# Kernel optimization log

Hardware: AMD Instinct MI355X
Metric: run time of the kernel (lower is better)

Reference implementation:

```python
import jax, jax.numpy as jnp
import numpy as np

DIM = 512
HEADS = 8
DEPTH = DIM // HEADS
DFF = 2048
EPS = 1e-3  # keras BatchNormalization default epsilon


def _dense_params(key, d_in, d_out, bias=True):
    k1, k2 = jax.random.split(key)
    lim = 1.0 / np.sqrt(d_in)
    W = jax.random.uniform(k1, (d_in, d_out), minval=-lim, maxval=lim, dtype=jnp.float32)
    if bias:
        b = jnp.zeros((d_out,), jnp.float32)
        return W, b
    return W


def _bn_params(key, d):
    k1, k2 = jax.random.split(key)
    gamma = 1.0 + 0.1 * jax.random.normal(k1, (d,), jnp.float32)
    beta = 0.1 * jax.random.normal(k2, (d,), jnp.float32)
    mean = 0.05 * jax.random.normal(jax.random.fold_in(key, 7), (d,), jnp.float32)
    var = jnp.ones((d,), jnp.float32)
    return gamma, beta, mean, var


def setup_inputs() -> dict:
    key = jax.random.key(0)
    ks = jax.random.split(key, 20)
    B, S_dec, S_enc = 32, 384, 384
    inp = {
        'enc_output': jax.random.normal(ks[0], (B, S_enc, DIM), jnp.float32),
        'x2': jax.random.normal(ks[1], (B, S_dec, DIM), jnp.float32),
    }
    # mha1 (self-attn) params
    for i, nm in enumerate(['q1', 'k1', 'v1', 'o1']):
        W, b = _dense_params(ks[2 + i], DIM, DIM)
        inp[f'W{nm}'], inp[f'b{nm}'] = W, b
    # mha2 (cross-attn) params
    for i, nm in enumerate(['q2', 'k2', 'v2', 'o2']):
        W, b = _dense_params(ks[6 + i], DIM, DIM)
        inp[f'W{nm}'], inp[f'b{nm}'] = W, b
    # FFN
    inp['Wff1'] = _dense_params(ks[10], DIM, DFF, bias=False)
    inp['Wff2'] = _dense_params(ks[11], DFF, DIM, bias=False)
    # 4 batchnorms
    for i in range(1, 5):
        g, be, m, v = _bn_params(ks[11 + i], DIM)
        inp[f'bn{i}_gamma'], inp[f'bn{i}_beta'] = g, be
        inp[f'bn{i}_mean'], inp[f'bn{i}_var'] = m, v
    return inp


def _split_heads(x):
    B, S, _ = x.shape
    return x.reshape(B, S, HEADS, DEPTH).transpose(0, 2, 1, 3)


def _mha(q_in, k_in, v_in, Wq, bq, Wk, bk, Wv, bv, Wo, bo, causal):
    q = _split_heads(q_in @ Wq + bq)
    k = _split_heads(k_in @ Wk + bk)
    v = _split_heads(v_in @ Wv + bv)
    logits = jnp.einsum('bhqd,bhkd->bhqk', q, k) / jnp.sqrt(jnp.float32(DEPTH))
    if causal:
        Sq, Sk = logits.shape[-2], logits.shape[-1]
        mask = jnp.tril(jnp.ones((Sq, Sk), bool))
        logits = jnp.where(mask, logits, jnp.finfo(logits.dtype).min)
    attn = jax.nn.softmax(logits, axis=-1)
    out = jnp.einsum('bhqk,bhkd->bhqd', attn, v)
    B, _, S, _ = out.shape
    out = out.transpose(0, 2, 1, 3).reshape(B, S, DIM)
    return out @ Wo + bo


def _bn(x, gamma, beta, mean, var):
    return (x - mean) * jax.lax.rsqrt(var + EPS) * gamma + beta


def reference(enc_output, x2,
              Wq1, bq1, Wk1, bk1, Wv1, bv1, Wo1, bo1,
              Wq2, bq2, Wk2, bk2, Wv2, bv2, Wo2, bo2,
              Wff1, Wff2,
              bn1_gamma, bn1_beta, bn1_mean, bn1_var,
              bn2_gamma, bn2_beta, bn2_mean, bn2_var,
              bn3_gamma, bn3_beta, bn3_mean, bn3_var,
              bn4_gamma, bn4_beta, bn4_mean, bn4_var):
    # self-attention with causal mask (dropout = identity)
    x = _mha(x2, x2, x2, Wq1, bq1, Wk1, bk1, Wv1, bv1, Wo1, bo1, causal=True)
    x = x + x2
    xn = _bn(x, bn1_gamma, bn1_beta, bn1_mean, bn1_var)
    y = _bn(enc_output, bn2_gamma, bn2_beta, bn2_mean, bn2_var)
    # cross-attention (no mask); residual adds x2 (as in source)
    x = _mha(xn, y, y, Wq2, bq2, Wk2, bk2, Wv2, bv2, Wo2, bo2, causal=False)
    x = x + x2
    cross_out = x
    x = _bn(x, bn3_gamma, bn3_beta, bn3_mean, bn3_var)
    x = jax.nn.relu(x @ Wff1) @ Wff2
    x = x + cross_out
    x = _bn(x, bn4_gamma, bn4_beta, bn4_mean, bn4_var)
    return x
```

## Files before the change

kernel.cpp:

```cpp
#include <hip/hip_runtime.h>
#include <cstdint>
#include <cstddef>

typedef __bf16 bf16;
typedef __bf16 bf16x8 __attribute__((ext_vector_type(8)));
typedef __bf16 bf16x4 __attribute__((ext_vector_type(4)));
typedef float  f32x4  __attribute__((ext_vector_type(4)));

#define B_   32
#define S_   384
#define D_   512
#define H_   8
#define DH_  64
#define DFF_ 2048
#define NTOK (B_*S_)

__device__ __forceinline__ void gload16(const void* g, void* l){
  __builtin_amdgcn_global_load_lds((__attribute__((address_space(1))) uint32_t*)(g),
                                   (__attribute__((address_space(3))) uint32_t*)(l), 16, 0, 0);
}

struct PrepArgs { const float* w8[8]; const float* wff1; const float* wff2; const float* bn[16]; };
__global__ __launch_bounds__(256) void prep_all(PrepArgs pa, bf16* Wt8, bf16* Wff1t, bf16* Wff2t,
                                                float* sc, float* sh){
  __shared__ float t[64][65];
  int id = blockIdx.x;
  if (id < 1024){
    const float* src; bf16* dst; int R, C, tr, tc;
    if (id < 512){
      int w = id >> 6, tl = id & 63;
      src = pa.w8[w]; dst = Wt8 + (size_t)w*262144; R = 512; C = 512;
      tr = (tl>>3)*64; tc = (tl&7)*64;
    } else if (id < 768){
      int tl = id - 512;
      src = pa.wff1; dst = Wff1t; R = 512; C = 2048;
      tr = (tl>>5)*64; tc = (tl&31)*64;
    } else {
      int tl = id - 768;
      src = pa.wff2; dst = Wff2t; R = 2048; C = 512;
      tr = (tl>>3)*64; tc = (tl&7)*64;
    }
    for (int i=threadIdx.x; i<4096; i+=256){ int r=i>>6, c=i&63; t[r][c] = src[(size_t)(tr+r)*C + tc+c]; }
    __syncthreads();
    for (int i=threadIdx.x; i<4096; i+=256){ int c=i>>6, r=i&63; dst[(size_t)(tc+c)*R + tr+r] = (bf16)t[r][c]; }
  } else {
    int t2 = id - 1024;
    int i = t2 >> 1, half = t2 & 1;
    int n = half*256 + threadIdx.x;
    float g = pa.bn[i*4+0][n], b = pa.bn[i*4+1][n], m = pa.bn[i*4+2][n], v = pa.bn[i*4+3][n];
    float s = g * rsqrtf(v + 1e-3f);
    sc[i*512+n] = s; sh[i*512+n] = b - m*s;
  }
}

__global__ __launch_bounds__(256) void cvt2(const float* __restrict__ enc, const float* __restrict__ x2,
                                            const float* __restrict__ sc, const float* __restrict__ sh,
                                            bf16* __restrict__ E2, bf16* __restrict__ X2b){
  size_t e0 = ((size_t)blockIdx.x*256 + threadIdx.x)*4;
  if (blockIdx.y == 0){
    int n0 = (int)(e0 & (D_-1));
    f32x4 xv = *(const f32x4*)(enc + e0);
    bf16x4 ov;
    #pragma unroll
    for (int j=0;j<4;j++) ov[j] = (bf16)(xv[j]*sc[n0+j] + sh[n0+j]);
    *(bf16x4*)(E2 + e0) = ov;
  } else {
    f32x4 xv = *(const f32x4*)(x2 + e0);
    bf16x4 ov;
    #pragma unroll
    for (int j=0;j<4;j++) ov[j] = (bf16)xv[j];
    *(bf16x4*)(X2b + e0) = ov;
  }
}

__global__ __launch_bounds__(256,3) void gemm_bt(
    const bf16* __restrict__ A, const bf16* __restrict__ Wt,
    const float* __restrict__ b0,
    const bf16* __restrict__ residb,
    const float* __restrict__ bsc, const float* __restrict__ bsh,
    bf16* __restrict__ o0, bf16* __restrict__ o1b,
    bf16* __restrict__ vt, int vseg,
    float* __restrict__ of, bf16* __restrict__ pre,
    int M, int N, int K, int relu, int mode)
{
  __shared__ bf16 As[2][64*64];
  __shared__ bf16 Bs[2][128*64];
  int nwg = gridDim.x;
  int cpx = nwg >> 3;
  int bid = blockIdx.x;
  int swz = (bid & 7)*cpx + (bid >> 3);
  int tiles_n = N >> 7;
  int tm = swz / tiles_n, tn = swz - tm*tiles_n;

  int tid = threadIdx.x, wave = tid>>6, lane = tid&63;
  int lhi = lane>>4, llo = lane&15;
  int lrow = lane>>3, lcol = lane&7;
  int wr = wave>>1, wc = wave&1;

  f32x4 acc[2][4];
  #pragma unroll
  for (int i=0;i<2;i++)
    #pragma unroll
    for (int j=0;j<4;j++) acc[i][j] = (f32x4){0.f,0.f,0.f,0.f};

  const bf16* Abase = A  + (size_t)(tm*64)  * K;
  const bf16* Bbase = Wt + (size_t)(tn*128) * K;

  int arow0 = wave*16, brow0 = wave*32;

  auto STAGE = [&](int buf, int kt){
    #pragma unroll
    for (int q=0;q<2;q++){
      int r = arow0 + q*8 + lrow;
      int s = lcol ^ (r&7);
      gload16(Abase + (size_t)r*K + kt + s*8, (char*)&As[buf][0] + wave*2048 + q*1024);
    }
    #pragma unroll
    for (int q=0;q<4;q++){
      int r = brow0 + q*8 + lrow;
      int s = lcol ^ (r&7);
      gload16(Bbase + (size_t)r*K + kt + s*8, (char*)&Bs[buf][0] + wave*4096 + q*1024);
    }
  };

  STAGE(0, 0);
  __syncthreads();
  int nt = K >> 6;
  int cur = 0;
  for (int t=0; t<nt; ++t){
    if (t+1 < nt) STAGE(cur^1, (t+1)<<6);
    #pragma unroll
    for (int ks=0; ks<2; ks++){
      bf16x8 af[2], bfr[4];
      #pragma unroll
      for (int i=0;i<2;i++){
        int row = wr*32 + i*16 + llo;
        int slot = (ks*4 + lhi) ^ (row&7);
        af[i] = *(const bf16x8*)&As[cur][row*64 + slot*8];
      }
      #pragma unroll
      for (int j=0;j<4;j++){
        int row = wc*64 + j*16 + llo;
        int slot = (ks*4 + lhi) ^ (row&7);
        bfr[j] = *(const bf16x8*)&Bs[cur][row*64 + slot*8];
      }
      #pragma unroll
      for (int i=0;i<2;i++)
        #pragma unroll
        for (int j=0;j<4;j++)
          acc[i][j] = __builtin_amdgcn_mfma_f32_16x16x32_bf16(af[i], bfr[j], acc[i][j], 0,0,0);
    }
    __syncthreads();
    cur ^= 1;
  }

  int m0 = tm*64 + wr*32, n0 = tn*128 + wc*64;
  #pragma unroll
  for (int i=0;i<2;i++){
    #pragma unroll
    for (int j=0;j<4;j++){
      int gn = n0 + j*16 + llo;
      float vv[4];
      #pragma unroll
      for (int rr=0;rr<4;rr++){
        int gm = m0 + i*16 + lhi*4 + rr;
        float v = acc[i][j][rr];
        if (b0) v += b0[gn & 511];
        if (residb) v += (float)residb[(size_t)gm*N + gn];
        vv[rr] = v;
      }
      int gm0 = m0 + i*16 + lhi*4;
      if (mode == 1){
        int seg = gn >> 9, cn = gn & 511;
        int h = cn >> 6, dd = cn & 63;
        int bb = gm0 / S_, ss0 = gm0 - bb*S_;
        if (seg == vseg){
          bf16x4 v4;
          #pragma unroll
          for (int rr=0;rr<4;rr++) v4[rr] = (bf16)vv[rr];
          *(bf16x4*)&vt[((size_t)(bb*H_ + h)*DH_ + dd)*S_ + ss0] = v4;
        } else {
          bf16* hp = (seg == 0) ? o0 : o1b;
          #pragma unroll
          for (int rr=0;rr<4;rr++)
            hp[(((size_t)(bb*H_ + h))*S_ + ss0 + rr)*DH_ + dd] = (bf16)vv[rr];
        }
      } else {
        #pragma unroll
        for (int rr=0;rr<4;rr++){
          int gm = gm0 + rr;
          float v = vv[rr];
          if (pre)  pre[(size_t)gm*N + gn] = (bf16)v;
          if (bsc)  v = v*bsc[gn & 511] + bsh[gn & 511];
          if (relu) v = fmaxf(v, 0.f);
          if (of) of[(size_t)gm*N + gn] = v;
          else    o0[(size_t)gm*N + gn] = (bf16)v;
        }
      }
    }
  }
}

__global__ __launch_bounds__(256,3) void gemm_bt2(
    const bf16* __restrict__ A, const bf16* __restrict__ A2, int tnA,
    const bf16* __restrict__ Wt,
    const float* __restrict__ b0, const float* __restrict__ b1, const float* __restrict__ b2,
    const bf16* __restrict__ residb,
    const float* __restrict__ bsc, const float* __restrict__ bsh,
    bf16* __restrict__ o0, bf16* __restrict__ o1b,
    bf16* __restrict__ vt, int vseg,
    float* __restrict__ of,
    int M, int N, int K, int relu, int mode)
{
  __shared__ bf16 As[3][128*32];
  __shared__ bf16 Bs[3][128*32];
  int nwg = gridDim.x;
  int cpx = nwg >> 3;
  int bid = blockIdx.x;
  int swz = (bid & 7)*cpx + (bid >> 3);
  int tiles_n = N >> 7;
  int tm = swz / tiles_n, tn = swz - tm*tiles_n;

  int tid = threadIdx.x, wave = tid>>6, lane = tid&63;
  int lhi = lane>>4, llo = lane&15;
  int srow = lane>>2, sslot = lane&3;
  int wr = wave>>1, wc = wave&1;

  f32x4 acc[4][4];
  #pragma unroll
  for (int i=0;i<4;i++)
    #pragma unroll
    for (int j=0;j<4;j++) acc[i][j] = (f32x4){0.f,0.f,0.f,0.f};

  const bf16* Asrc = (A2 && tn >= tnA) ? A2 : A;
  const bf16* Abase = Asrc + (size_t)(tm*128) * K;
  const bf16* Bbase = Wt   + (size_t)(tn*128) * K;

  auto STAGE = [&](int buf, int kt){
    #pragma unroll
    for (int q=0;q<2;q++){
      int r = wave*32 + q*16 + srow;
      int s = sslot ^ ((r>>1)&3);
      gload16(Abase + (size_t)r*K + kt + s*8, (char*)&As[buf][0] + wave*2048 + q*1024);
    }
    #pragma unroll
    for (int q=0;q<2;q++){
      int r = wave*32 + q*16 + srow;
      int s = sslot ^ ((r>>1)&3);
      gload16(Bbase + (size_t)r*K + kt + s*8, (char*)&Bs[buf][0] + wave*2048 + q*1024);
    }
  };

  int nt = K >> 5;
  STAGE(0, 0);
  STAGE(1, 32);
  int cur = 0, st = 2;
  for (int t=0; t<nt; ++t){
    if (t+1 < nt) asm volatile("s_waitcnt vmcnt(4)" ::: "memory");
    else          asm volatile("s_waitcnt vmcnt(0)" ::: "memory");
    __builtin_amdgcn_s_barrier();
    asm volatile("" ::: "memory");
    if (t+2 < nt){
      STAGE(st, (t+2)<<5);
      st = (st==2) ? 0 : st+1;
    }
    bf16x8 af[4], bfr[4];
    #pragma unroll
    for (int i=0;i<4;i++){
      int row = wr*64 + i*16 + llo;
      int slot = lhi ^ ((row>>1)&3);
      af[i] = *(const bf16x8*)&As[cur][row*32 + slot*8];
    }
    #pragma unroll
    for (int j=0;j<4;j++){
      int row = wc*64 + j*16 + llo;
      int slot = lhi ^ ((row>>1)&3);
      bfr[j] = *(const bf16x8*)&Bs[cur][row*32 + slot*8];
    }
    #pragma unroll
    for (int i=0;i<4;i++)
      #pragma unroll
      for (int j=0;j<4;j++)
        acc[i][j] = __builtin_amdgcn_mfma_f32_16x16x32_bf16(af[i], bfr[j], acc[i][j], 0,0,0);
    cur = (cur==2) ? 0 : cur+1;
  }

  int m0 = tm*128 + wr*64, n0 = tn*128 + wc*64;
  #pragma unroll
  for (int i=0;i<4;i++){
    #pragma unroll
    for (int j=0;j<4;j++){
      int gn = n0 + j*16 + llo;
      float vv[4];
      #pragma unroll
      for (int rr=0;rr<4;rr++){
        int gm = m0 + i*16 + lhi*4 + rr;
        float v = acc[i][j][rr];
        if (b0){
          const float* bp = (gn < 512) ? b0 : ((gn < 1024) ? b1 : b2);
          v += bp[gn & 511];
        }
        if (residb) v += (float)residb[(size_t)gm*N + gn];
        vv[rr] = v;
      }
      int gm0 = m0 + i*16 + lhi*4;
      if (mode == 1){
        int seg = gn >> 9, cn = gn & 511;
        int h = cn >> 6, dd = cn & 63;
        int bb = gm0 / S_, ss0 = gm0 - bb*S_;
        if (seg == vseg){
          bf16x4 v4;
          #pragma unroll
          for (int rr=0;rr<4;rr++) v4[rr] = (bf16)vv[rr];
          *(bf16x4*)&vt[((size_t)(bb*H_ + h)*DH_ + dd)*S_ + ss0] = v4;
        } else {
          bf16* hp = (seg == 0) ? o0 : o1b;
          #pragma unroll
          for (int rr=0;rr<4;rr++)
            hp[(((size_t)(bb*H_ + h))*S_ + ss0 + rr)*DH_ + dd] = (bf16)vv[rr];
        }
      } else {
        #pragma unroll
        for (int rr=0;rr<4;rr++){
          int gm = gm0 + rr;
          float v = vv[rr];
          if (bsc)  v = v*bsc[gn & 511] + bsh[gn & 511];
          if (relu) v = fmaxf(v, 0.f);
          if (of) of[(size_t)gm*N + gn] = v;
          else    o0[(size_t)gm*N + gn] = (bf16)v;
        }
      }
    }
  }
}

__global__ __launch_bounds__(256,4) void attn(
    const bf16* __restrict__ Q, const bf16* __restrict__ Kx,
    const bf16* __restrict__ Vt, bf16* __restrict__ out, int causal)
{
  __shared__ bf16 Ks[64*64];
  __shared__ bf16 Vs[64*64];
  __shared__ bf16 Ps[4][16*64];
  int bid = blockIdx.x;
  int bh = bid & 255;
  int qb = bid >> 8;
  int b = bh >> 3, h = bh & 7;
  int tid = threadIdx.x, wave = tid>>6, lane = tid&63;
  int lhi = lane>>4, llo = lane&15;
  int l7 = llo & 7;
  const bf16* Qb = Q  + (size_t)bh*S_*DH_;
  const bf16* Kb = Kx + (size_t)bh*S_*DH_;
  const bf16* Vb = Vt + (size_t)bh*DH_*S_;

  bf16x8 qf[2];
  #pragma unroll
  for (int f=0; f<2; f++)
    qf[f] = *(const bf16x8*)&Qb[(size_t)(qb*64 + wave*16 + llo)*DH_ + f*32 + lhi*8];

  f32x4 oacc[4];
  #pragma unroll
  for (int f=0; f<4; f++) oacc[f] = (f32x4){0.f,0.f,0.f,0.f};
  float mrow[4], lrow4[4];
  #pragma unroll
  for (int r=0;r<4;r++){ mrow[r] = -1e9f; lrow4[r] = 0.f; }

  int KT = causal ? (qb+1) : (S_/64);

  int srow0 = tid>>3, sslot = tid&7;
  bf16x8 kreg[2], vreg[2];

  auto issue = [&](int kb){
    const bf16* kt0 = Kb + (size_t)kb*64*DH_;
    #pragma unroll
    for (int s=0;s<2;s++){
      int row = s*32 + srow0;
      kreg[s] = *(const bf16x8*)&kt0[(size_t)row*64 + sslot*8];
      vreg[s] = *(const bf16x8*)&Vb[(size_t)row*S_ + (size_t)kb*64 + sslot*8];
    }
  };
  issue(0);

  for (int kb=0; kb<KT; kb++){
    #pragma unroll
    for (int s=0;s<2;s++){
      int row = s*32 + srow0;
      int sl = sslot ^ (row&7);
      *(bf16x8*)&Ks[row*64 + sl*8] = kreg[s];
      *(bf16x8*)&Vs[row*64 + sl*8] = vreg[s];
    }
    __syncthreads();

    f32x4 sc[4];
    #pragma unroll
    for (int f=0; f<4; f++){
      f32x4 z = (f32x4){0.f,0.f,0.f,0.f};
      #pragma unroll
      for (int ks=0; ks<2; ks++){
        int row = f*16 + llo;
        int slot = (ks*4 + lhi) ^ (row&7);
        bf16x8 kf = *(const bf16x8*)&Ks[row*64 + slot*8];
        z = __builtin_amdgcn_mfma_f32_16x16x32_bf16(qf[ks], kf, z, 0,0,0);
      }
      sc[f] = z;
    }
    #pragma unroll
    for (int f=0; f<4; f++)
      #pragma unroll
      for (int r=0;r<4;r++){
        float v = sc[f][r]*0.125f;
        if (causal && kb==KT-1){
          int gcol = kb*64 + f*16 + llo;
          int grow = qb*64 + wave*16 + lhi*4 + r;
          if (gcol > grow) v = -1e9f;
        }
        sc[f][r] = v;
      }

    float alpha[4], psum[4];
    #pragma unroll
    for (int r=0;r<4;r++){
      float vm = fmaxf(fmaxf(sc[0][r],sc[1][r]), fmaxf(sc[2][r],sc[3][r]));
      #pragma unroll
      for (int msk=1; msk<16; msk<<=1) vm = fmaxf(vm, __shfl_xor(vm, msk));
      float mn = fmaxf(mrow[r], vm);
      alpha[r] = __expf(mrow[r]-mn);
      mrow[r]  = mn;
      psum[r]  = 0.f;
    }
    #pragma unroll
    for (int f=0; f<4; f++)
      #pragma unroll
      for (int r=0;r<4;r++){
        float p = __expf(sc[f][r]-mrow[r]);
        psum[r] += p;
        int row = lhi*4 + r;
        int slot = (f*2 + (llo>>3)) ^ (row&7);
        Ps[wave][row*64 + slot*8 + l7] = (bf16)p;
      }
    #pragma unroll
    for (int r=0;r<4;r++){
      float s = psum[r];
      #pragma unroll
      for (int msk=1; msk<16; msk<<=1) s += __shfl_xor(s, msk);
      lrow4[r] = lrow4[r]*alpha[r] + s;
      #pragma unroll
      for (int f=0; f<4; f++) oacc[f][r] *= alpha[r];
    }

    if (kb+1 < KT) issue(kb+1);

    asm volatile("s_waitcnt lgkmcnt(0)" ::: "memory");
    __builtin_amdgcn_sched_barrier(0);

    #pragma unroll
    for (int ks=0; ks<2; ks++){
      int pslot = (ks*4 + lhi) ^ l7;
      bf16x8 pf = *(const bf16x8*)&Ps[wave][llo*64 + pslot*8];
      #pragma unroll
      for (int f2=0; f2<4; f2++){
        int row = f2*16 + llo;
        int slot = (ks*4 + lhi) ^ (row&7);
        bf16x8 vf = *(const bf16x8*)&Vs[row*64 + slot*8];
        oacc[f2] = __builtin_amdgcn_mfma_f32_16x16x32_bf16(pf, vf, oacc[f2], 0,0,0);
      }
    }
    __syncthreads();
  }

  int qg = qb*64 + wave*16;
  #pragma unroll
  for (int f2=0; f2<4; f2++)
    #pragma unroll
    for (int r=0;r<4;r++){
      int row = qg + lhi*4 + r;
      int dd  = f2*16 + llo;
      out[((size_t)(b*S_ + row))*D_ + h*DH_ + dd] = (bf16)(oacc[f2][r] / lrow4[r]);
    }
}

extern "C" void kernel_launch(void* const* d_in, const int* in_sizes, int n_in,
                              void* d_out, int out_size, void* d_ws, size_t ws_size,
                              hipStream_t stream)
{
  (void)in_sizes; (void)n_in; (void)out_size; (void)ws_size;
  const float* enc = (const float*)d_in[0];
  const float* x2  = (const float*)d_in[1];
  const float* bq1 = (const float*)d_in[3];
  const float* bk1 = (const float*)d_in[5];
  const float* bv1 = (const float*)d_in[7];
  const float* bo1 = (const float*)d_in[9];
  const float* bq2 = (const float*)d_in[11];
  const float* bk2 = (const float*)d_in[13];
  const float* bv2 = (const float*)d_in[15];
  const float* bo2 = (const float*)d_in[17];
  float* outp = (float*)d_out;

  char* ws = (char*)d_ws;
  size_t off = 0;
  auto alloc = [&](size_t bytes)->void*{ void* p = ws + off; off += (bytes+255)&~(size_t)255; return p; };
  bf16* Wt8   = (bf16*)alloc((size_t)8*512*512*2);
  bf16* Wff1t = (bf16*)alloc((size_t)DFF_*D_*2);
  bf16* Wff2t = (bf16*)alloc((size_t)D_*DFF_*2);
  float* bnsc = (float*)alloc(4*512*4);
  float* bnsh = (float*)alloc(4*512*4);
  size_t actB = (size_t)NTOK*D_*2;
  bf16* X2b  = (bf16*)alloc(actB);
  bf16* Abuf = (bf16*)alloc(actB);
  bf16* Bbuf = (bf16*)alloc(actB);
  bf16* Cbuf = (bf16*)alloc(actB);
  bf16* Dv   = (bf16*)alloc(actB);
  bf16* E1   = (bf16*)alloc(actB);
  bf16* E2   = (bf16*)alloc(actB);
  bf16* E3   = E2;
  bf16* Fbuf = Abuf;

  bf16* Wtq1 = Wt8 + 0*262144;
  bf16* Wto1 = Wt8 + 3*262144;
  bf16* Wtq2 = Wt8 + 4*262144;
  bf16* Wto2 = Wt8 + 7*262144;

  PrepArgs pa;
  pa.w8[0]=(const float*)d_in[2];  pa.w8[1]=(const float*)d_in[4];
  pa.w8[2]=(const float*)d_in[6];  pa.w8[3]=(const float*)d_in[8];
  pa.w8[4]=(const float*)d_in[10]; pa.w8[5]=(const float*)d_in[12];
  pa.w8[6]=(const float*)d_in[14]; pa.w8[7]=(const float*)d_in[16];
  pa.wff1=(const float*)d_in[18];  pa.wff2=(const float*)d_in[19];
  for (int i=0;i<16;i++) pa.bn[i] = (const float*)d_in[20+i];
  prep_all<<<1032,256,0,stream>>>(pa, Wt8, Wff1t, Wff2t, bnsc, bnsh);
  cvt2<<<dim3(NTOK*D_/4/256, 2),256,0,stream>>>(enc, x2, bnsc+512, bnsh+512, E2, X2b);

  auto gemm = [&](const bf16* Am, const bf16* W, const float* bb0,
                  const bf16* residb, const float* sc, const float* sh,
                  bf16* oo0, float* of, bf16* pre, int N, int K, int relu){
    gemm_bt<<<(NTOK/64)*(N/128), 256, 0, stream>>>(Am, W, bb0, residb, sc, sh,
                                                   oo0, nullptr, nullptr, -1, of, pre,
                                                   NTOK, N, K, relu, 0);
  };
  auto gemm2 = [&](const bf16* Am, const bf16* A2, int tnA, const bf16* W,
                   const float* bb0, const float* bb1, const float* bb2,
                   const bf16* residb, const float* sc, const float* sh,
                   bf16* oo0, bf16* oo1, bf16* vt, int vseg, float* of,
                   int N, int K, int relu, int mode){
    gemm_bt2<<<(NTOK/128)*(N/128), 256, 0, stream>>>(Am, A2, tnA, W, bb0, bb1, bb2,
                                                     residb, sc, sh, oo0, oo1, vt, vseg, of,
                                                     NTOK, N, K, relu, mode);
  };

  gemm2(X2b, nullptr, 0, Wtq1, bq1, bk1, bv1, nullptr, nullptr, nullptr,
        Abuf, Bbuf, Dv, 2, nullptr, 1536, 512, 0, 1);
  attn<<<(S_/64)*B_*H_, 256, 0, stream>>>(Abuf, Bbuf, Dv, Cbuf, 1);
  gemm(Cbuf, Wto1, bo1, X2b, bnsc+0, bnsh+0, E1, nullptr, nullptr, 512, 512, 0);

  gemm2(E1, E2, 4, Wtq2, bq2, bk2, bv2, nullptr, nullptr, nullptr,
        Abuf, Bbuf, Dv, 2, nullptr, 1536, 512, 0, 1);
  attn<<<(S_/64)*B_*H_, 256, 0, stream>>>(Abuf, Bbuf, Dv, Cbuf, 0);
  gemm(Cbuf, Wto2, bo2, X2b, bnsc+2*512, bnsh+2*512, E1, nullptr, E3, 512, 512, 0);

  gemm2(E1, nullptr, 0, Wff1t, nullptr, nullptr, nullptr, nullptr, nullptr, nullptr,
        Fbuf, nullptr, nullptr, -1, nullptr, DFF_, 512, 1, 0);
  gemm2(Fbuf, nullptr, 0, Wff2t, nullptr, nullptr, nullptr, E3, bnsc+3*512, bnsh+3*512,
        nullptr, nullptr, nullptr, -1, outp, 512, DFF_, 0, 0);
}
```

Before: 334.9 us.

## Simplify gemm kernels: double-buffer gemm_bt2, route FFN2 through 64-row gemm_bt

Splits the epilogues so gemm_bt handles only row-major outputs with residual, batchnorm and fp32 output, while gemm_bt2 handles only the QKV/FFN1 paths. gemm_bt2 moves from a triple-buffered LDS pipeline with manual vmcnt waits to a simpler double buffer with __syncthreads, which cuts LDS use so launch bounds can go up to 4 blocks per CU. The FFN2 GEMM (K=2048, N=512) now runs on the 64x128-tile gemm_bt, which launches more workgroups. The cost is less prefetch depth in gemm_bt2, so global load latency may be exposed more often.

```diff
diff --git a/kernel.cpp b/kernel.cpp
--- a/kernel.cpp
+++ b/kernel.cpp
@@ -78,10 +78,9 @@
     const float* __restrict__ b0,
     const bf16* __restrict__ residb,
     const float* __restrict__ bsc, const float* __restrict__ bsh,
-    bf16* __restrict__ o0, bf16* __restrict__ o1b,
-    bf16* __restrict__ vt, int vseg,
+    bf16* __restrict__ o0,
     float* __restrict__ of, bf16* __restrict__ pre,
-    int M, int N, int K, int relu, int mode)
+    int M, int N, int K, int relu)
 {
   __shared__ bf16 As[2][64*64];
   __shared__ bf16 Bs[2][128*64];
@@ -160,13 +159,112 @@
     #pragma unroll
     for (int j=0;j<4;j++){
       int gn = n0 + j*16 + llo;
-      float vv[4];
       #pragma unroll
       for (int rr=0;rr<4;rr++){
         int gm = m0 + i*16 + lhi*4 + rr;
         float v = acc[i][j][rr];
         if (b0) v += b0[gn & 511];
         if (residb) v += (float)residb[(size_t)gm*N + gn];
+        if (pre)  pre[(size_t)gm*N + gn] = (bf16)v;
+        if (bsc)  v = v*bsc[gn & 511] + bsh[gn & 511];
+        if (relu) v = fmaxf(v, 0.f);
+        if (of) of[(size_t)gm*N + gn] = v;
+        else    o0[(size_t)gm*N + gn] = (bf16)v;
+      }
+    }
+  }
+}
+
+__global__ __launch_bounds__(256,4) void gemm_bt2(
+    const bf16* __restrict__ A, const bf16* __restrict__ A2, int tnA,
+    const bf16* __restrict__ Wt,
+    const float* __restrict__ b0, const float* __restrict__ b1, const float* __restrict__ b2,
+    bf16* __restrict__ o0, bf16* __restrict__ o1b,
+    bf16* __restrict__ vt, int vseg,
+    int M, int N, int K, int relu, int mode)
+{
+  __shared__ bf16 As[2][128*32];
+  __shared__ bf16 Bs[2][128*32];
+  int nwg = gridDim.x;
+  int cpx = nwg >> 3;
+  int bid = blockIdx.x;
+  int swz = (bid & 7)*cpx + (bid >> 3);
+  int tiles_n = N >> 7;
+  int tm = swz / tiles_n, tn = swz - tm*tiles_n;
+
+  int tid = threadIdx.x, wave = tid>>6, lane = tid&63;
+  int lhi = lane>>4, llo = lane&15;
+  int srow = lane>>2, sslot = lane&3;
+  int wr = wave>>1, wc = wave&1;
+
+  f32x4 acc[4][4];
+  #pragma unroll
+  for (int i=0;i<4;i++)
+    #pragma unroll
+    for (int j=0;j<4;j++) acc[i][j] = (f32x4){0.f,0.f,0.f,0.f};
+
+  const bf16* Asrc = (A2 && tn >= tnA) ? A2 : A;
+  const bf16* Abase = Asrc + (size_t)(tm*128) * K;
+  const bf16* Bbase = Wt   + (size_t)(tn*128) * K;
+
+  auto STAGE = [&](int buf, int kt){
+    #pragma unroll
+    for (int q=0;q<2;q++){
+      int r = wave*32 + q*16 + srow;
+      int s = sslot ^ ((r>>1)&3);
+      gload16(Abase + (size_t)r*K + kt + s*8, (char*)&As[buf][0] + wave*2048 + q*1024);
+    }
+    #pragma unroll
+    for (int q=0;q<2;q++){
+      int r = wave*32 + q*16 + srow;
+      int s = sslot ^ ((r>>1)&3);
+      gload16(Bbase + (size_t)r*K + kt + s*8, (char*)&Bs[buf][0] + wave*2048 + q*1024);
+    }
+  };
+
+  STAGE(0, 0);
+  __syncthreads();
+  int nt = K >> 5;
+  int cur = 0;
+  for (int t=0; t<nt; ++t){
+    if (t+1 < nt) STAGE(cur^1, (t+1)<<5);
+    bf16x8 af[4], bfr[4];
+    #pragma unroll
+    for (int i=0;i<4;i++){
+      int row = wr*64 + i*16 + llo;
+      int slot = lhi ^ ((row>>1)&3);
+      af[i] = *(const bf16x8*)&As[cur][row*32 + slot*8];
+    }
+    #pragma unroll
+    for (int j=0;j<4;j++){
+      int row = wc*64 + j*16 + llo;
+      int slot = lhi ^ ((row>>1)&3);
+      bfr[j] = *(const bf16x8*)&Bs[cur][row*32 + slot*8];
+    }
+    #pragma unroll
+    for (int i=0;i<4;i++)
+      #pragma unroll
+      for (int j=0;j<4;j++)
+        acc[i][j] = __builtin_amdgcn_mfma_f32_16x16x32_bf16(af[i], bfr[j], acc[i][j], 0,0,0);
+    __syncthreads();
+    cur ^= 1;
+  }
+
+  int m0 = tm*128 + wr*64, n0 = tn*128 + wc*64;
+  #pragma unroll
+  for (int i=0;i<4;i++){
+    #pragma unroll
+    for (int j=0;j<4;j++){
+      int gn = n0 + j*16 + llo;
+      float vv[4];
+      #pragma unroll
+      for (int rr=0;rr<4;rr++){
+        int gm = m0 + i*16 + lhi*4 + rr;
+        float v = acc[i][j][rr];
+        if (b0){
+          const float* bp = (gn < 512) ? b0 : ((gn < 1024) ? b1 : b2);
+          v += bp[gn & 511];
+        }
         vv[rr] = v;
       }
       int gm0 = m0 + i*16 + lhi*4;
@@ -190,144 +288,8 @@
         for (int rr=0;rr<4;rr++){
           int gm = gm0 + rr;
           float v = vv[rr];
-          if (pre)  pre[(size_t)gm*N + gn] = (bf16)v;
-          if (bsc)  v = v*bsc[gn & 511] + bsh[gn & 511];
           if (relu) v = fmaxf(v, 0.f);
-          if (of) of[(size_t)gm*N + gn] = v;
-          else    o0[(size_t)gm*N + gn] = (bf16)v;
-        }
-      }
-    }
-  }
-}
-
-__global__ __launch_bounds__(256,3) void gemm_bt2(
-    const bf16* __restrict__ A, const bf16* __restrict__ A2, int tnA,
-    const bf16* __restrict__ Wt,
-    const float* __restrict__ b0, const float* __restrict__ b1, const float* __restrict__ b2,
-    const bf16* __restrict__ residb,
-    const float* __restrict__ bsc, const float* __restrict__ bsh,
-    bf16* __restrict__ o0, bf16* __restrict__ o1b,
-    bf16* __restrict__ vt, int vseg,
-    float* __restrict__ of,
-    int M, int N, int K, int relu, int mode)
-{
-  __shared__ bf16 As[3][128*32];
-  __shared__ bf16 Bs[3][128*32];
-  int nwg = gridDim.x;
-  int cpx = nwg >> 3;
-  int bid = blockIdx.x;
-  int swz = (bid & 7)*cpx + (bid >> 3);
-  int tiles_n = N >> 7;
-  int tm = swz / tiles_n, tn = swz - tm*tiles_n;
-
-  int tid = threadIdx.x, wave = tid>>6, lane = tid&63;
-  int lhi = lane>>4, llo = lane&15;
-  int srow = lane>>2, sslot = lane&3;
-  int wr = wave>>1, wc = wave&1;
-
-  f32x4 acc[4][4];
-  #pragma unroll
-  for (int i=0;i<4;i++)
-    #pragma unroll
-    for (int j=0;j<4;j++) acc[i][j] = (f32x4){0.f,0.f,0.f,0.f};
-
-  const bf16* Asrc = (A2 && tn >= tnA) ? A2 : A;
-  const bf16* Abase = Asrc + (size_t)(tm*128) * K;
-  const bf16* Bbase = Wt   + (size_t)(tn*128) * K;
-
-  auto STAGE = [&](int buf, int kt){
-    #pragma unroll
-    for (int q=0;q<2;q++){
-      int r = wave*32 + q*16 + srow;
-      int s = sslot ^ ((r>>1)&3);
-      gload16(Abase + (size_t)r*K + kt + s*8, (char*)&As[buf][0] + wave*2048 + q*1024);
-    }
-    #pragma unroll
-    for (int q=0;q<2;q++){
-      int r = wave*32 + q*16 + srow;
-      int s = sslot ^ ((r>>1)&3);
-      gload16(Bbase + (size_t)r*K + kt + s*8, (char*)&Bs[buf][0] + wave*2048 + q*1024);
-    }
-  };
-
-  int nt = K >> 5;
-  STAGE(0, 0);
-  STAGE(1, 32);
-  int cur = 0, st = 2;
-  for (int t=0; t<nt; ++t){
-    if (t+1 < nt) asm volatile("s_waitcnt vmcnt(4)" ::: "memory");
-    else          asm volatile("s_waitcnt vmcnt(0)" ::: "memory");
-    __builtin_amdgcn_s_barrier();
-    asm volatile("" ::: "memory");
-    if (t+2 < nt){
-      STAGE(st, (t+2)<<5);
-      st = (st==2) ? 0 : st+1;
-    }
-    bf16x8 af[4], bfr[4];
-    #pragma unroll
-    for (int i=0;i<4;i++){
-      int row = wr*64 + i*16 + llo;
-      int slot = lhi ^ ((row>>1)&3);
-      af[i] = *(const bf16x8*)&As[cur][row*32 + slot*8];
-    }
-    #pragma unroll
-    for (int j=0;j<4;j++){
-      int row = wc*64 + j*16 + llo;
-      int slot = lhi ^ ((row>>1)&3);
-      bfr[j] = *(const bf16x8*)&Bs[cur][row*32 + slot*8];
-    }
-    #pragma unroll
-    for (int i=0;i<4;i++)
-      #pragma unroll
-      for (int j=0;j<4;j++)
-        acc[i][j] = __builtin_amdgcn_mfma_f32_16x16x32_bf16(af[i], bfr[j], acc[i][j], 0,0,0);
-    cur = (cur==2) ? 0 : cur+1;
-  }
-
-  int m0 = tm*128 + wr*64, n0 = tn*128 + wc*64;
-  #pragma unroll
-  for (int i=0;i<4;i++){
-    #pragma unroll
-    for (int j=0;j<4;j++){
-      int gn = n0 + j*16 + llo;
-      float vv[4];
-      #pragma unroll
-      for (int rr=0;rr<4;rr++){
-        int gm = m0 + i*16 + lhi*4 + rr;
-        float v = acc[i][j][rr];
-        if (b0){
-          const float* bp = (gn < 512) ? b0 : ((gn < 1024) ? b1 : b2);
-          v += bp[gn & 511];
-        }
-        if (residb) v += (float)residb[(size_t)gm*N + gn];
-        vv[rr] = v;
-      }
-      int gm0 = m0 + i*16 + lhi*4;
-      if (mode == 1){
-        int seg = gn >> 9, cn = gn & 511;
-        int h = cn >> 6, dd = cn & 63;
-        int bb = gm0 / S_, ss0 = gm0 - bb*S_;
-        if (seg == vseg){
-          bf16x4 v4;
-          #pragma unroll
-          for (int rr=0;rr<4;rr++) v4[rr] = (bf16)vv[rr];
-          *(bf16x4*)&vt[((size_t)(bb*H_ + h)*DH_ + dd)*S_ + ss0] = v4;
-        } else {
-          bf16* hp = (seg == 0) ? o0 : o1b;
-          #pragma unroll
-          for (int rr=0;rr<4;rr++)
-            hp[(((size_t)(bb*H_ + h))*S_ + ss0 + rr)*DH_ + dd] = (bf16)vv[rr];
-        }
-      } else {
-        #pragma unroll
-        for (int rr=0;rr<4;rr++){
-          int gm = gm0 + rr;
-          float v = vv[rr];
-          if (bsc)  v = v*bsc[gn & 511] + bsh[gn & 511];
-          if (relu) v = fmaxf(v, 0.f);
-          if (of) of[(size_t)gm*N + gn] = v;
-          else    o0[(size_t)gm*N + gn] = (bf16)v;
+          o0[(size_t)gm*N + gn] = (bf16)v;
         }
       }
     }
@@ -533,31 +495,26 @@
                   const bf16* residb, const float* sc, const float* sh,
                   bf16* oo0, float* of, bf16* pre, int N, int K, int relu){
     gemm_bt<<<(NTOK/64)*(N/128), 256, 0, stream>>>(Am, W, bb0, residb, sc, sh,
-                                                   oo0, nullptr, nullptr, -1, of, pre,
-                                                   NTOK, N, K, relu, 0);
+                                                   oo0, of, pre, NTOK, N, K, relu);
   };
   auto gemm2 = [&](const bf16* Am, const bf16* A2, int tnA, const bf16* W,
                    const float* bb0, const float* bb1, const float* bb2,
-                   const bf16* residb, const float* sc, const float* sh,
-                   bf16* oo0, bf16* oo1, bf16* vt, int vseg, float* of,
+                   bf16* oo0, bf16* oo1, bf16* vt, int vseg,
                    int N, int K, int relu, int mode){
     gemm_bt2<<<(NTOK/128)*(N/128), 256, 0, stream>>>(Am, A2, tnA, W, bb0, bb1, bb2,
-                                                     residb, sc, sh, oo0, oo1, vt, vseg, of,
+                                                     oo0, oo1, vt, vseg,
                                                      NTOK, N, K, relu, mode);
   };
 
-  gemm2(X2b, nullptr, 0, Wtq1, bq1, bk1, bv1, nullptr, nullptr, nullptr,
-        Abuf, Bbuf, Dv, 2, nullptr, 1536, 512, 0, 1);
+  gemm2(X2b, nullptr, 0, Wtq1, bq1, bk1, bv1, Abuf, Bbuf, Dv, 2, 1536, 512, 0, 1);
   attn<<<(S_/64)*B_*H_, 256, 0, stream>>>(Abuf, Bbuf, Dv, Cbuf, 1);
   gemm(Cbuf, Wto1, bo1, X2b, bnsc+0, bnsh+0, E1, nullptr, nullptr, 512, 512, 0);
 
-  gemm2(E1, E2, 4, Wtq2, bq2, bk2, bv2, nullptr, nullptr, nullptr,
-        Abuf, Bbuf, Dv, 2, nullptr, 1536, 512, 0, 1);
+  gemm2(E1, E2, 4, Wtq2, bq2, bk2, bv2, Abuf, Bbuf, Dv, 2, 1536, 512, 0, 1);
   attn<<<(S_/64)*B_*H_, 256, 0, stream>>>(Abuf, Bbuf, Dv, Cbuf, 0);
   gemm(Cbuf, Wto2, bo2, X2b, bnsc+2*512, bnsh+2*512, E1, nullptr, E3, 512, 512, 0);
 
-  gemm2(E1, nullptr, 0, Wff1t, nullptr, nullptr, nullptr, nullptr, nullptr, nullptr,
-        Fbuf, nullptr, nullptr, -1, nullptr, DFF_, 512, 1, 0);
-  gemm2(Fbuf, nullptr, 0, Wff2t, nullptr, nullptr, nullptr, E3, bnsc+3*512, bnsh+3*512,
-        nullptr, nullptr, nullptr, -1, outp, 512, DFF_, 0, 0);
-}
+  gemm2(E1, nullptr, 0, Wff1t, nullptr, nullptr, nullptr, Fbuf, nullptr, nullptr, -1,
+        DFF_, 512, 1, 0);
+  gemm(Fbuf, Wff2t, nullptr, E3, bnsc+3*512, bnsh+3*512, nullptr, outp, nullptr, 512, DFF_, 0);
+}
```

Result: faster. 306.5 us (median of 2 runs) (-8.5%).
